# Optimization experiments

Measured on AMD Instinct MI355X. Metric: run time of the kernel, lower is better.

## Reference

```python
import jax, jax.numpy as jnp
import numpy as np

GROUP = 64      # SVDQuant hard-coded group size
QMAX = 7.0      # symmetric int4: values in [-8, 7], scale = max|x| / 7
EPS = 1e-8


def setup_inputs() -> dict:
    key = jax.random.key(0)
    k0, k1, k2, k3, k4 = jax.random.split(key, 5)
    T, K, N, R = 4096, 4096, 4096, 32  # tokens, in_features, out_features, rank

    x = jax.random.normal(k0, (T, K), jnp.float32)

    # Full-precision weight, decomposed offline into low-rank + int4 residual
    w = jax.random.normal(k1, (N, K), jnp.float32) * 0.02
    proj_down = jax.random.normal(k2, (K, R), jnp.float32) * 0.02  # x @ proj_down -> [T, R]
    proj_up = jax.random.normal(k3, (R, N), jnp.float32) * 0.02    # [T, R] @ proj_up -> [T, N]
    residual = w - (proj_down @ proj_up).T  # [N, K]

    # Symmetric per-group int4 quantization of the residual weight
    rg = residual.reshape(N, K // GROUP, GROUP)
    wscales = jnp.maximum(jnp.max(jnp.abs(rg), axis=-1) / QMAX, EPS)  # [N, K/G]
    q_w = jnp.clip(jnp.round(rg / wscales[..., None]), -8, 7).astype(jnp.int8).reshape(N, K)

    smooth = jnp.ones((K,), jnp.float32)  # load_from_replicated sets smooth to ones
    bias = jax.random.normal(k4, (N,), jnp.float32) * 0.02
    return {
        "x": x,
        "q_w": q_w,
        "wscales": wscales,
        "proj_down": proj_down,
        "proj_up": proj_up,
        "smooth": smooth,
        "bias": bias,
    }


def reference(x, q_w, wscales, proj_down, proj_up, smooth, bias):
    T, K = x.shape
    N = q_w.shape[0]

    # smoothing (identity here, per load_from_replicated)
    xs = x * smooth

    # low-rank SVD correction branch (full precision)
    lr = (xs @ proj_down) @ proj_up  # [T, N]

    # W4A4 branch: symmetric per-token per-group int4 activation quantization
    xg = xs.reshape(T, K // GROUP, GROUP)
    ascales = jnp.maximum(jnp.max(jnp.abs(xg), axis=-1) / QMAX, EPS)  # [T, K/G]
    q_x = jnp.clip(jnp.round(xg / ascales[..., None]), -8.0, 7.0)
    x_dq = (q_x * ascales[..., None]).reshape(T, K)  # dequantized activations

    # dequantize int4 weights with per-(out_channel, group) scales
    w_dq = (q_w.astype(jnp.float32).reshape(N, K // GROUP, GROUP)
            * wscales[..., None]).reshape(N, K)

    # fused dequant-matmul + low-rank add + bias
    return lr + x_dq @ w_dq.T + bias
```

## Files before the change

kernel.cpp:

```cpp
#include <hip/hip_runtime.h>
#include <hip/hip_bf16.h>
#include <stdint.h>

#define Tdim 4096
#define Ndim 4096
#define Kdim 4096
#define K2   4160

using f32x4  = __attribute__((ext_vector_type(4))) float;
using bf16x8 = __attribute__((ext_vector_type(8))) short;

__device__ inline ushort f2bf(float f) {
  union { float f; unsigned u; } v; v.f = f;
  unsigned lsb = (v.u >> 16) & 1u;
  v.u += 0x7fffu + lsb;
  return (ushort)(v.u >> 16);
}

__device__ inline void async16(const void* g, void* l) {
  __builtin_amdgcn_global_load_lds(
      (const __attribute__((address_space(1))) unsigned int*)g,
      (__attribute__((address_space(3))) unsigned int*)l, 16, 0, 0);
}

__global__ __launch_bounds__(256) void prep_pdT_kernel(
    const float* __restrict__ pd, ushort* __restrict__ pdT) {
  const int idx = blockIdx.x * 256 + threadIdx.x;
  const int n = idx >> 12;
  const int k = idx & 4095;
  pdT[(size_t)n * Kdim + k] = f2bf(pd[(size_t)k * 32 + n]);
}

__global__ __launch_bounds__(256) void lowrank_gemm_kernel(
    const float* __restrict__ x, const float* __restrict__ smooth,
    const ushort* __restrict__ pdT, float* __restrict__ partials) {
  __shared__ ushort sA[128 * 32];
  const int tid  = threadIdx.x;
  const int lane = tid & 63;
  const int wave = tid >> 6;
  const int tok0 = blockIdx.x * 128;
  const int kc0  = blockIdx.y * 512;
  const int fr  = lane & 15;
  const int fkq = lane >> 4;
  const int fk  = fkq * 8;
  const int srow = tid >> 3;
  const int scol = (tid & 7) * 4;

  f32x4 acc[2][2] = {};

  for (int step = 0; step < 16; ++step) {
    const int k0 = kc0 + step * 32;
#pragma unroll
    for (int p = 0; p < 4; ++p) {
      const int r = srow + p * 32;
      const float4 xv = *(const float4*)&x[(size_t)(tok0 + r) * Kdim + k0 + scol];
      const float4 sm = *(const float4*)&smooth[k0 + scol];
      ushort4 o;
      o.x = f2bf(xv.x * sm.x);
      o.y = f2bf(xv.y * sm.y);
      o.z = f2bf(xv.z * sm.z);
      o.w = f2bf(xv.w * sm.w);
      *(ushort4*)&sA[r * 32 + scol] = o;
    }
    __syncthreads();
    bf16x8 af[2], bfr[2];
#pragma unroll
    for (int i = 0; i < 2; ++i)
      af[i] = *(const bf16x8*)&sA[(wave * 32 + i * 16 + fr) * 32 + fk];
#pragma unroll
    for (int j = 0; j < 2; ++j)
      bfr[j] = *(const bf16x8*)&pdT[(size_t)(j * 16 + fr) * Kdim + k0 + fk];
#pragma unroll
    for (int i = 0; i < 2; ++i)
#pragma unroll
      for (int j = 0; j < 2; ++j)
        acc[i][j] = __builtin_amdgcn_mfma_f32_16x16x32_bf16(af[i], bfr[j], acc[i][j], 0, 0, 0);
    __syncthreads();
  }

  float* P = partials + (size_t)blockIdx.y * Tdim * 32;
#pragma unroll
  for (int i = 0; i < 2; ++i) {
    const int row0 = tok0 + wave * 32 + i * 16 + fkq * 4;
#pragma unroll
    for (int j = 0; j < 2; ++j) {
      const int col = j * 16 + fr;
#pragma unroll
      for (int r = 0; r < 4; ++r)
        P[(size_t)(row0 + r) * 32 + col] = acc[i][j][r];
    }
  }
}

__global__ __launch_bounds__(256) void reduce_tail_A_kernel(
    const float* __restrict__ partials, ushort* __restrict__ A) {
  const int idx = blockIdx.x * 256 + threadIdx.x;
  const int token = idx >> 6, c = idx & 63;
  ushort v = 0;
  if (c < 32) {
    float s = 0.f;
#pragma unroll
    for (int p = 0; p < 8; ++p)
      s += partials[(size_t)p * Tdim * 32 + (size_t)token * 32 + c];
    v = f2bf(s);
  }
  A[(size_t)token * K2 + Kdim + c] = v;
}

__global__ __launch_bounds__(256) void quant_x_kernel(
    const float* __restrict__ x, const float* __restrict__ smooth,
    ushort* __restrict__ A) {
  const int g = blockIdx.x * 256 + threadIdx.x;
  const int token = g >> 10;
  const int k = (g & 1023) * 4;
  const float4 xv = *(const float4*)&x[(size_t)token * Kdim + k];
  const float4 sm = *(const float4*)&smooth[k];
  const float v0 = xv.x * sm.x, v1 = xv.y * sm.y, v2 = xv.z * sm.z, v3 = xv.w * sm.w;
  float a = fmaxf(fmaxf(fabsf(v0), fabsf(v1)), fmaxf(fabsf(v2), fabsf(v3)));
  a = fmaxf(a, __shfl_xor(a, 1));
  a = fmaxf(a, __shfl_xor(a, 2));
  a = fmaxf(a, __shfl_xor(a, 4));
  a = fmaxf(a, __shfl_xor(a, 8));
  const float s = fmaxf(a / 7.0f, 1e-8f);
  const float q0 = fminf(fmaxf(rintf(v0 / s), -8.f), 7.f);
  const float q1 = fminf(fmaxf(rintf(v1 / s), -8.f), 7.f);
  const float q2 = fminf(fmaxf(rintf(v2 / s), -8.f), 7.f);
  const float q3 = fminf(fmaxf(rintf(v3 / s), -8.f), 7.f);
  ushort4 o;
  o.x = f2bf(q0 * s);
  o.y = f2bf(q1 * s);
  o.z = f2bf(q2 * s);
  o.w = f2bf(q3 * s);
  *(ushort4*)&A[(size_t)token * K2 + k] = o;
}

__global__ __launch_bounds__(256) void tail_B_kernel(
    const float* __restrict__ pu, ushort* __restrict__ B) {
  const int idx = blockIdx.x * 256 + threadIdx.x;
  const int n = idx >> 6, c = idx & 63;
  ushort v = 0;
  if (c < 32) v = f2bf(pu[(size_t)c * Ndim + n]);
  B[(size_t)n * K2 + Kdim + c] = v;
}

__global__ __launch_bounds__(256) void dequant_w_kernel(
    const int* __restrict__ qw, const float* __restrict__ wsc,
    ushort* __restrict__ B) {
  const size_t idx = ((size_t)blockIdx.x * 256 + threadIdx.x) * 8;
  const int n = (int)(idx >> 12);
  const int k = (int)(idx & 4095);
  const float s = wsc[n * 64 + (k >> 6)];
  const int4 q0 = *(const int4*)(qw + idx);
  const int4 q1 = *(const int4*)(qw + idx + 4);
  ushort4 o0, o1;
  o0.x = f2bf((float)q0.x * s);
  o0.y = f2bf((float)q0.y * s);
  o0.z = f2bf((float)q0.z * s);
  o0.w = f2bf((float)q0.w * s);
  o1.x = f2bf((float)q1.x * s);
  o1.y = f2bf((float)q1.y * s);
  o1.z = f2bf((float)q1.z * s);
  o1.w = f2bf((float)q1.w * s);
  ushort* dst = B + (size_t)n * K2 + k;
  *(ushort4*)dst = o0;
  *(ushort4*)(dst + 4) = o1;
}

__global__ __launch_bounds__(256) void gemm_kernel(
    const ushort* __restrict__ A, const ushort* __restrict__ B,
    const float* __restrict__ bias, float* __restrict__ C) {
  __shared__ ushort sA[128 * 32];
  __shared__ ushort sB[128 * 32];
  const int tid  = threadIdx.x;
  const int lane = tid & 63;
  const int wave = tid >> 6;
  const int wr = (wave >> 1) * 64;
  const int wc = (wave & 1) * 64;
  const int fr = lane & 15;
  const int fk = (lane >> 4) * 8;
  const size_t arow0 = (size_t)blockIdx.x * 128;
  const size_t brow0 = (size_t)blockIdx.y * 128;
  const int srow = tid >> 2;
  const int skc  = (tid & 3) * 8;

  f32x4 acc[4][4] = {};

  for (int k0 = 0; k0 < K2; k0 += 32) {
    const ushort* gA0 = A + (arow0 + srow) * K2 + k0 + skc;
    const ushort* gB0 = B + (brow0 + srow) * K2 + k0 + skc;
    async16(gA0,                    &sA[tid * 8]);
    async16(gA0 + (size_t)64 * K2,  &sA[(tid + 256) * 8]);
    async16(gB0,                    &sB[tid * 8]);
    async16(gB0 + (size_t)64 * K2,  &sB[(tid + 256) * 8]);
    __syncthreads();

    bf16x8 af[4], bfr[4];
#pragma unroll
    for (int i = 0; i < 4; ++i)
      af[i] = *(const bf16x8*)&sA[(wr + i * 16 + fr) * 32 + fk];
#pragma unroll
    for (int j = 0; j < 4; ++j)
      bfr[j] = *(const bf16x8*)&sB[(wc + j * 16 + fr) * 32 + fk];
#pragma unroll
    for (int i = 0; i < 4; ++i)
#pragma unroll
      for (int j = 0; j < 4; ++j)
        acc[i][j] = __builtin_amdgcn_mfma_f32_16x16x32_bf16(af[i], bfr[j], acc[i][j], 0, 0, 0);
    __syncthreads();
  }

  const int rq = (lane >> 4) * 4;
#pragma unroll
  for (int j = 0; j < 4; ++j) {
    const size_t col = brow0 + wc + j * 16 + fr;
    const float bv = bias[col];
#pragma unroll
    for (int i = 0; i < 4; ++i) {
      const size_t row = arow0 + wr + i * 16 + rq;
#pragma unroll
      for (int r = 0; r < 4; ++r)
        C[(row + r) * Ndim + col] = acc[i][j][r] + bv;
    }
  }
}

extern "C" void kernel_launch(void* const* d_in, const int* in_sizes, int n_in,
                              void* d_out, int out_size, void* d_ws, size_t ws_size,
                              hipStream_t stream) {
  const float* x      = (const float*)d_in[0];
  const int*   qw     = (const int*)d_in[1];
  const float* wsc    = (const float*)d_in[2];
  const float* pd     = (const float*)d_in[3];
  const float* pu     = (const float*)d_in[4];
  const float* smooth = (const float*)d_in[5];
  const float* bias   = (const float*)d_in[6];
  float* out = (float*)d_out;

  const size_t abytes = (size_t)Tdim * K2 * 2;
  ushort* A   = (ushort*)d_ws;
  ushort* B   = (ushort*)((char*)d_ws + abytes);
  ushort* pdT = (ushort*)((char*)d_ws + 2 * abytes);
  float*  part= (float*)((char*)d_ws + 2 * abytes + 262144);

  hipLaunchKernelGGL(prep_pdT_kernel,    dim3(512),    dim3(256), 0, stream, pd, pdT);
  hipLaunchKernelGGL(quant_x_kernel,     dim3(16384),  dim3(256), 0, stream, x, smooth, A);
  hipLaunchKernelGGL(lowrank_gemm_kernel,dim3(32, 8),  dim3(256), 0, stream, x, smooth, pdT, part);
  hipLaunchKernelGGL(reduce_tail_A_kernel,dim3(1024),  dim3(256), 0, stream, part, A);
  hipLaunchKernelGGL(dequant_w_kernel,   dim3(8192),   dim3(256), 0, stream, qw, wsc, B);
  hipLaunchKernelGGL(tail_B_kernel,      dim3(1024),   dim3(256), 0, stream, pu, B);
  hipLaunchKernelGGL(gemm_kernel,        dim3(32, 32), dim3(256), 0, stream, A, B, bias, out);
}
```

Measured before the change: 381.0 us.

## Fuse activation quant with low-rank GEMM, merge prep kernels, unroll GEMM K-loop

Activation quantization is folded into the low-rank down-projection kernel, so x is read from global memory once per tile. The kernel writes the dequantized bf16 A tile from shared memory and reads proj_down directly, which removes the separate transpose kernel. Weight dequant, partial reduction and proj_up tail packing are merged into one launch that dispatches on block index, cutting seven launches to three. The main GEMM now stages two 32-wide K slices per barrier, halving the number of syncs in exchange for more LDS use and uncoalesced strided pd loads in the fused kernel.

```diff
diff --git a/kernel.cpp b/kernel.cpp
--- a/kernel.cpp
+++ b/kernel.cpp
@@ -17,64 +17,97 @@
   return (ushort)(v.u >> 16);
 }
 
+__device__ inline unsigned pack2(float a, float b) {
+  return (unsigned)f2bf(a) | ((unsigned)f2bf(b) << 16);
+}
+
+__device__ inline float qd(float v, float s) {
+  return fminf(fmaxf(rintf(v / s), -8.f), 7.f) * s;
+}
+
 __device__ inline void async16(const void* g, void* l) {
   __builtin_amdgcn_global_load_lds(
       (const __attribute__((address_space(1))) unsigned int*)g,
       (__attribute__((address_space(3))) unsigned int*)l, 16, 0, 0);
 }
 
-__global__ __launch_bounds__(256) void prep_pdT_kernel(
-    const float* __restrict__ pd, ushort* __restrict__ pdT) {
-  const int idx = blockIdx.x * 256 + threadIdx.x;
-  const int n = idx >> 12;
-  const int k = idx & 4095;
-  pdT[(size_t)n * Kdim + k] = f2bf(pd[(size_t)k * 32 + n]);
-}
-
-__global__ __launch_bounds__(256) void lowrank_gemm_kernel(
+__global__ __launch_bounds__(256) void prep_a_kernel(
     const float* __restrict__ x, const float* __restrict__ smooth,
-    const ushort* __restrict__ pdT, float* __restrict__ partials) {
-  __shared__ ushort sA[128 * 32];
+    const float* __restrict__ pd, ushort* __restrict__ A,
+    float* __restrict__ partials) {
+  __shared__ __attribute__((aligned(16))) ushort sXS[128 * 136];
+  __shared__ __attribute__((aligned(16))) ushort sQ[128 * 136];
   const int tid  = threadIdx.x;
   const int lane = tid & 63;
   const int wave = tid >> 6;
-  const int tok0 = blockIdx.x * 128;
-  const int kc0  = blockIdx.y * 512;
   const int fr  = lane & 15;
   const int fkq = lane >> 4;
   const int fk  = fkq * 8;
-  const int srow = tid >> 3;
-  const int scol = (tid & 7) * 4;
+  const int tok0 = blockIdx.x * 128;
+  const int kc0  = blockIdx.y * 512;
+  const int r = tid >> 1;
+  const int g = tid & 1;
+  const int srow2 = tid >> 2;
+  const int scol2 = (tid & 3) * 8;
 
   f32x4 acc[2][2] = {};
 
-  for (int step = 0; step < 16; ++step) {
-    const int k0 = kc0 + step * 32;
-#pragma unroll
-    for (int p = 0; p < 4; ++p) {
-      const int r = srow + p * 32;
-      const float4 xv = *(const float4*)&x[(size_t)(tok0 + r) * Kdim + k0 + scol];
-      const float4 sm = *(const float4*)&smooth[k0 + scol];
-      ushort4 o;
-      o.x = f2bf(xv.x * sm.x);
-      o.y = f2bf(xv.y * sm.y);
-      o.z = f2bf(xv.z * sm.z);
-      o.w = f2bf(xv.w * sm.w);
-      *(ushort4*)&sA[r * 32 + scol] = o;
-    }
-    __syncthreads();
-    bf16x8 af[2], bfr[2];
-#pragma unroll
-    for (int i = 0; i < 2; ++i)
-      af[i] = *(const bf16x8*)&sA[(wave * 32 + i * 16 + fr) * 32 + fk];
-#pragma unroll
-    for (int j = 0; j < 2; ++j)
-      bfr[j] = *(const bf16x8*)&pdT[(size_t)(j * 16 + fr) * Kdim + k0 + fk];
-#pragma unroll
-    for (int i = 0; i < 2; ++i)
-#pragma unroll
-      for (int j = 0; j < 2; ++j)
-        acc[i][j] = __builtin_amdgcn_mfma_f32_16x16x32_bf16(af[i], bfr[j], acc[i][j], 0, 0, 0);
+  for (int c = 0; c < 4; ++c) {
+    const int kbase = kc0 + c * 128;
+    const int kcol  = g * 64;
+    const float4* xp = (const float4*)&x[(size_t)(tok0 + r) * Kdim + kbase + kcol];
+    const float4* sp = (const float4*)&smooth[kbase + kcol];
+    float4 v[16];
+#pragma unroll
+    for (int q = 0; q < 16; ++q) {
+      float4 xv = xp[q], sm = sp[q];
+      v[q].x = xv.x * sm.x; v[q].y = xv.y * sm.y;
+      v[q].z = xv.z * sm.z; v[q].w = xv.w * sm.w;
+    }
+    float a = 0.f;
+#pragma unroll
+    for (int q = 0; q < 16; ++q)
+      a = fmaxf(a, fmaxf(fmaxf(fabsf(v[q].x), fabsf(v[q].y)),
+                         fmaxf(fabsf(v[q].z), fabsf(v[q].w))));
+    const float s = fmaxf(a / 7.0f, 1e-8f);
+#pragma unroll
+    for (int q2 = 0; q2 < 8; ++q2) {
+      const float4 v0 = v[2 * q2], v1 = v[2 * q2 + 1];
+      uint4 wx, wq;
+      wx.x = pack2(v0.x, v0.y);           wx.y = pack2(v0.z, v0.w);
+      wx.z = pack2(v1.x, v1.y);           wx.w = pack2(v1.z, v1.w);
+      wq.x = pack2(qd(v0.x, s), qd(v0.y, s)); wq.y = pack2(qd(v0.z, s), qd(v0.w, s));
+      wq.z = pack2(qd(v1.x, s), qd(v1.y, s)); wq.w = pack2(qd(v1.z, s), qd(v1.w, s));
+      *(uint4*)&sXS[r * 136 + kcol + q2 * 8] = wx;
+      *(uint4*)&sQ [r * 136 + kcol + q2 * 8] = wq;
+    }
+    __syncthreads();
+
+#pragma unroll
+    for (int kk = 0; kk < 4; ++kk) {
+      bf16x8 af0 = *(const bf16x8*)&sXS[(wave * 32 + fr) * 136 + kk * 32 + fk];
+      bf16x8 af1 = *(const bf16x8*)&sXS[(wave * 32 + 16 + fr) * 136 + kk * 32 + fk];
+      bf16x8 b0, b1;
+#pragma unroll
+      for (int e = 0; e < 8; ++e) {
+        const size_t kr = (size_t)(kbase + kk * 32 + fk + e) * 32;
+        b0[e] = (short)f2bf(pd[kr + fr]);
+        b1[e] = (short)f2bf(pd[kr + 16 + fr]);
+      }
+      acc[0][0] = __builtin_amdgcn_mfma_f32_16x16x32_bf16(af0, b0, acc[0][0], 0, 0, 0);
+      acc[0][1] = __builtin_amdgcn_mfma_f32_16x16x32_bf16(af0, b1, acc[0][1], 0, 0, 0);
+      acc[1][0] = __builtin_amdgcn_mfma_f32_16x16x32_bf16(af1, b0, acc[1][0], 0, 0, 0);
+      acc[1][1] = __builtin_amdgcn_mfma_f32_16x16x32_bf16(af1, b1, acc[1][1], 0, 0, 0);
+    }
+
+#pragma unroll
+    for (int h = 0; h < 2; ++h) {
+      const int rr = srow2 + h * 64;
+#pragma unroll
+      for (int u = 0; u < 4; ++u)
+        *(uint4*)&A[(size_t)(tok0 + rr) * K2 + kbase + scol2 + u * 32] =
+            *(const uint4*)&sQ[rr * 136 + scol2 + u * 32];
+    }
     __syncthreads();
   }
 
@@ -86,91 +119,56 @@
     for (int j = 0; j < 2; ++j) {
       const int col = j * 16 + fr;
 #pragma unroll
-      for (int r = 0; r < 4; ++r)
-        P[(size_t)(row0 + r) * 32 + col] = acc[i][j][r];
-    }
-  }
-}
-
-__global__ __launch_bounds__(256) void reduce_tail_A_kernel(
-    const float* __restrict__ partials, ushort* __restrict__ A) {
-  const int idx = blockIdx.x * 256 + threadIdx.x;
-  const int token = idx >> 6, c = idx & 63;
-  ushort v = 0;
-  if (c < 32) {
-    float s = 0.f;
-#pragma unroll
-    for (int p = 0; p < 8; ++p)
-      s += partials[(size_t)p * Tdim * 32 + (size_t)token * 32 + c];
-    v = f2bf(s);
-  }
-  A[(size_t)token * K2 + Kdim + c] = v;
-}
-
-__global__ __launch_bounds__(256) void quant_x_kernel(
-    const float* __restrict__ x, const float* __restrict__ smooth,
-    ushort* __restrict__ A) {
-  const int g = blockIdx.x * 256 + threadIdx.x;
-  const int token = g >> 10;
-  const int k = (g & 1023) * 4;
-  const float4 xv = *(const float4*)&x[(size_t)token * Kdim + k];
-  const float4 sm = *(const float4*)&smooth[k];
-  const float v0 = xv.x * sm.x, v1 = xv.y * sm.y, v2 = xv.z * sm.z, v3 = xv.w * sm.w;
-  float a = fmaxf(fmaxf(fabsf(v0), fabsf(v1)), fmaxf(fabsf(v2), fabsf(v3)));
-  a = fmaxf(a, __shfl_xor(a, 1));
-  a = fmaxf(a, __shfl_xor(a, 2));
-  a = fmaxf(a, __shfl_xor(a, 4));
-  a = fmaxf(a, __shfl_xor(a, 8));
-  const float s = fmaxf(a / 7.0f, 1e-8f);
-  const float q0 = fminf(fmaxf(rintf(v0 / s), -8.f), 7.f);
-  const float q1 = fminf(fmaxf(rintf(v1 / s), -8.f), 7.f);
-  const float q2 = fminf(fmaxf(rintf(v2 / s), -8.f), 7.f);
-  const float q3 = fminf(fmaxf(rintf(v3 / s), -8.f), 7.f);
-  ushort4 o;
-  o.x = f2bf(q0 * s);
-  o.y = f2bf(q1 * s);
-  o.z = f2bf(q2 * s);
-  o.w = f2bf(q3 * s);
-  *(ushort4*)&A[(size_t)token * K2 + k] = o;
-}
-
-__global__ __launch_bounds__(256) void tail_B_kernel(
-    const float* __restrict__ pu, ushort* __restrict__ B) {
-  const int idx = blockIdx.x * 256 + threadIdx.x;
-  const int n = idx >> 6, c = idx & 63;
-  ushort v = 0;
-  if (c < 32) v = f2bf(pu[(size_t)c * Ndim + n]);
-  B[(size_t)n * K2 + Kdim + c] = v;
-}
-
-__global__ __launch_bounds__(256) void dequant_w_kernel(
+      for (int rr = 0; rr < 4; ++rr)
+        P[(size_t)(row0 + rr) * 32 + col] = acc[i][j][rr];
+    }
+  }
+}
+
+__global__ __launch_bounds__(256) void wprep_kernel(
     const int* __restrict__ qw, const float* __restrict__ wsc,
-    ushort* __restrict__ B) {
-  const size_t idx = ((size_t)blockIdx.x * 256 + threadIdx.x) * 8;
-  const int n = (int)(idx >> 12);
-  const int k = (int)(idx & 4095);
-  const float s = wsc[n * 64 + (k >> 6)];
-  const int4 q0 = *(const int4*)(qw + idx);
-  const int4 q1 = *(const int4*)(qw + idx + 4);
-  ushort4 o0, o1;
-  o0.x = f2bf((float)q0.x * s);
-  o0.y = f2bf((float)q0.y * s);
-  o0.z = f2bf((float)q0.z * s);
-  o0.w = f2bf((float)q0.w * s);
-  o1.x = f2bf((float)q1.x * s);
-  o1.y = f2bf((float)q1.y * s);
-  o1.z = f2bf((float)q1.z * s);
-  o1.w = f2bf((float)q1.w * s);
-  ushort* dst = B + (size_t)n * K2 + k;
-  *(ushort4*)dst = o0;
-  *(ushort4*)(dst + 4) = o1;
+    const float* __restrict__ partials, const float* __restrict__ pu,
+    ushort* __restrict__ A, ushort* __restrict__ B) {
+  const int bid = blockIdx.x;
+  if (bid < 8192) {
+    const size_t idx = ((size_t)bid * 256 + threadIdx.x) * 8;
+    const int n = (int)(idx >> 12);
+    const int k = (int)(idx & 4095);
+    const float s = wsc[n * 64 + (k >> 6)];
+    const int4 q0 = *(const int4*)(qw + idx);
+    const int4 q1 = *(const int4*)(qw + idx + 4);
+    uint4 o;
+    o.x = pack2((float)q0.x * s, (float)q0.y * s);
+    o.y = pack2((float)q0.z * s, (float)q0.w * s);
+    o.z = pack2((float)q1.x * s, (float)q1.y * s);
+    o.w = pack2((float)q1.z * s, (float)q1.w * s);
+    *(uint4*)(B + (size_t)n * K2 + k) = o;
+  } else if (bid < 8192 + 1024) {
+    const int idx = (bid - 8192) * 256 + threadIdx.x;
+    const int token = idx >> 6, c = idx & 63;
+    ushort v = 0;
+    if (c < 32) {
+      float s = 0.f;
+#pragma unroll
+      for (int p = 0; p < 8; ++p)
+        s += partials[(size_t)p * Tdim * 32 + (size_t)token * 32 + c];
+      v = f2bf(s);
+    }
+    A[(size_t)token * K2 + Kdim + c] = v;
+  } else {
+    const int idx = (bid - 9216) * 256 + threadIdx.x;
+    const int n = idx >> 6, c = idx & 63;
+    ushort v = 0;
+    if (c < 32) v = f2bf(pu[(size_t)c * Ndim + n]);
+    B[(size_t)n * K2 + Kdim + c] = v;
+  }
 }
 
 __global__ __launch_bounds__(256) void gemm_kernel(
     const ushort* __restrict__ A, const ushort* __restrict__ B,
     const float* __restrict__ bias, float* __restrict__ C) {
-  __shared__ ushort sA[128 * 32];
-  __shared__ ushort sB[128 * 32];
+  __shared__ __attribute__((aligned(16))) ushort sA[2 * 128 * 32];
+  __shared__ __attribute__((aligned(16))) ushort sB[2 * 128 * 32];
   const int tid  = threadIdx.x;
   const int lane = tid & 63;
   const int wave = tid >> 6;
@@ -183,29 +181,37 @@
   const int srow = tid >> 2;
   const int skc  = (tid & 3) * 8;
 
+  const ushort* gA = A + (arow0 + srow) * K2 + skc;
+  const ushort* gB = B + (brow0 + srow) * K2 + skc;
+
   f32x4 acc[4][4] = {};
 
-  for (int k0 = 0; k0 < K2; k0 += 32) {
-    const ushort* gA0 = A + (arow0 + srow) * K2 + k0 + skc;
-    const ushort* gB0 = B + (brow0 + srow) * K2 + k0 + skc;
-    async16(gA0,                    &sA[tid * 8]);
-    async16(gA0 + (size_t)64 * K2,  &sA[(tid + 256) * 8]);
-    async16(gB0,                    &sB[tid * 8]);
-    async16(gB0 + (size_t)64 * K2,  &sB[(tid + 256) * 8]);
-    __syncthreads();
-
-    bf16x8 af[4], bfr[4];
-#pragma unroll
-    for (int i = 0; i < 4; ++i)
-      af[i] = *(const bf16x8*)&sA[(wr + i * 16 + fr) * 32 + fk];
-#pragma unroll
-    for (int j = 0; j < 4; ++j)
-      bfr[j] = *(const bf16x8*)&sB[(wc + j * 16 + fr) * 32 + fk];
-#pragma unroll
-    for (int i = 0; i < 4; ++i)
+  for (int k0 = 0; k0 < K2; k0 += 64) {
+#pragma unroll
+    for (int p = 0; p < 2; ++p) {
+      async16(gA + p * 32,                   &sA[p * 4096 + tid * 8]);
+      async16(gA + p * 32 + (size_t)64 * K2, &sA[p * 4096 + (tid + 256) * 8]);
+      async16(gB + p * 32,                   &sB[p * 4096 + tid * 8]);
+      async16(gB + p * 32 + (size_t)64 * K2, &sB[p * 4096 + (tid + 256) * 8]);
+    }
+    gA += 64; gB += 64;
+    __syncthreads();
+
+#pragma unroll
+    for (int kk = 0; kk < 2; ++kk) {
+      bf16x8 af[4], bfr[4];
+#pragma unroll
+      for (int i = 0; i < 4; ++i)
+        af[i] = *(const bf16x8*)&sA[kk * 4096 + (wr + i * 16 + fr) * 32 + fk];
 #pragma unroll
       for (int j = 0; j < 4; ++j)
-        acc[i][j] = __builtin_amdgcn_mfma_f32_16x16x32_bf16(af[i], bfr[j], acc[i][j], 0, 0, 0);
+        bfr[j] = *(const bf16x8*)&sB[kk * 4096 + (wc + j * 16 + fr) * 32 + fk];
+#pragma unroll
+      for (int i = 0; i < 4; ++i)
+#pragma unroll
+        for (int j = 0; j < 4; ++j)
+          acc[i][j] = __builtin_amdgcn_mfma_f32_16x16x32_bf16(af[i], bfr[j], acc[i][j], 0, 0, 0);
+    }
     __syncthreads();
   }
 
@@ -237,16 +243,11 @@
   float* out = (float*)d_out;
 
   const size_t abytes = (size_t)Tdim * K2 * 2;
-  ushort* A   = (ushort*)d_ws;
-  ushort* B   = (ushort*)((char*)d_ws + abytes);
-  ushort* pdT = (ushort*)((char*)d_ws + 2 * abytes);
-  float*  part= (float*)((char*)d_ws + 2 * abytes + 262144);
-
-  hipLaunchKernelGGL(prep_pdT_kernel,    dim3(512),    dim3(256), 0, stream, pd, pdT);
-  hipLaunchKernelGGL(quant_x_kernel,     dim3(16384),  dim3(256), 0, stream, x, smooth, A);
-  hipLaunchKernelGGL(lowrank_gemm_kernel,dim3(32, 8),  dim3(256), 0, stream, x, smooth, pdT, part);
-  hipLaunchKernelGGL(reduce_tail_A_kernel,dim3(1024),  dim3(256), 0, stream, part, A);
-  hipLaunchKernelGGL(dequant_w_kernel,   dim3(8192),   dim3(256), 0, stream, qw, wsc, B);
-  hipLaunchKernelGGL(tail_B_kernel,      dim3(1024),   dim3(256), 0, stream, pu, B);
-  hipLaunchKernelGGL(gemm_kernel,        dim3(32, 32), dim3(256), 0, stream, A, B, bias, out);
-}
+  ushort* A    = (ushort*)d_ws;
+  ushort* B    = (ushort*)((char*)d_ws + abytes);
+  float*  part = (float*)((char*)d_ws + 2 * abytes);
+
+  hipLaunchKernelGGL(prep_a_kernel, dim3(32, 8),  dim3(256), 0, stream, x, smooth, pd, A, part);
+  hipLaunchKernelGGL(wprep_kernel,  dim3(10240),  dim3(256), 0, stream, qw, wsc, part, pu, A, B);
+  hipLaunchKernelGGL(gemm_kernel,   dim3(32, 32), dim3(256), 0, stream, A, B, bias, out);
+}
```

New measurement: 374.4 us. About the same (-1.7%).
